# Kernel optimization log

Hardware: AMD Instinct MI355X
Metric: run time of the kernel (lower is better)

The kernel has to match this reference:

```python
import jax, jax.numpy as jnp
import numpy as np
import math

STRIDE = 32
CTR_CLAMP = 32.0
SCALE_CLAMP = math.log(1000.0 / 16)  # DEFAULT_SCALE_CLAMP
CONF_THRESH = 0.05
NMS_THRESH = 0.6
TOPK = 1000
NUM_CLASSES = 80
CLASS_OFFSET = 1.0e5  # separates classes so one IoU pass == per-class NMS


def setup_inputs() -> dict:
    key = jax.random.key(0)
    k1, k2 = jax.random.split(key)
    fmp_h, fmp_w = 100, 100
    A = 5
    M = fmp_h * fmp_w * A  # 50000 candidates
    cls_pred = jax.random.normal(k1, (M, NUM_CLASSES), dtype=jnp.float32)
    reg_pred = jax.random.normal(k2, (M, 4), dtype=jnp.float32)
    anchor_size = jnp.array([[32, 32], [64, 64], [128, 128], [256, 256], [512, 512]], dtype=jnp.float32)
    return {"cls_pred": cls_pred, "reg_pred": reg_pred, "anchor_size": anchor_size,
            "fmp_h": fmp_h, "fmp_w": fmp_w}


def _generate_anchors(anchor_size, fmp_h, fmp_w):
    # anchors laid out as [H*W, A, 4] -> [M, 4], matching torch.meshgrid order
    ys, xs = jnp.meshgrid(jnp.arange(fmp_h, dtype=jnp.float32),
                          jnp.arange(fmp_w, dtype=jnp.float32), indexing="ij")
    xy = (jnp.stack([xs, ys], axis=-1).reshape(-1, 2) + 0.5) * STRIDE  # [HW, 2]
    A = anchor_size.shape[0]
    anchor_xy = jnp.repeat(xy[:, None, :], A, axis=1)                   # [HW, A, 2]
    anchor_wh = jnp.broadcast_to(anchor_size[None], (xy.shape[0], A, 2))
    return jnp.concatenate([anchor_xy, anchor_wh], axis=-1).reshape(-1, 4)  # [M, 4]


def _decode_boxes(anchors, reg):
    # anchors/reg: [K, 4] (cx, cy, w, h) / (dx, dy, dw, dh)
    ctr_off = jnp.clip(reg[:, :2] * anchors[:, 2:], -CTR_CLAMP, CTR_CLAMP)
    ctr_xy = anchors[:, :2] + ctr_off
    wh = anchors[:, 2:] * jnp.exp(jnp.minimum(reg[:, 2:], SCALE_CLAMP))
    return jnp.concatenate([ctr_xy - 0.5 * wh, ctr_xy + 0.5 * wh], axis=-1)  # x1y1x2y2


def _greedy_nms_keep(boxes, valid):
    # boxes: [K, 4] already score-sorted descending; valid: [K] bool
    x1, y1, x2, y2 = boxes[:, 0], boxes[:, 1], boxes[:, 2], boxes[:, 3]
    areas = (x2 - x1) * (y2 - y1)
    xx1 = jnp.maximum(x1[:, None], x1[None, :])
    yy1 = jnp.maximum(y1[:, None], y1[None, :])
    xx2 = jnp.minimum(x2[:, None], x2[None, :])
    yy2 = jnp.minimum(y2[:, None], y2[None, :])
    inter = jnp.maximum(1e-28, xx2 - xx1) * jnp.maximum(1e-28, yy2 - yy1)
    iou = inter / (areas[:, None] + areas[None, :] - inter + 1e-14)  # [K, K]
    idxs = jnp.arange(boxes.shape[0])

    def body(i, keep):
        suppress = keep[i] & (iou[i] > NMS_THRESH) & (idxs > i)
        return keep & ~suppress

    return jax.lax.fori_loop(0, boxes.shape[0], body, valid)


def reference(cls_pred, reg_pred, anchor_size, fmp_h, fmp_w):
    anchors = _generate_anchors(anchor_size, fmp_h, fmp_w)  # [M, 4]
    probs = jax.nn.sigmoid(cls_pred)                        # [M, C]
    scores = probs.max(axis=-1)
    labels = probs.argmax(axis=-1)
    # top-k candidates (lax.top_k returns scores sorted descending)
    scores, idx = jax.lax.top_k(scores, TOPK)
    labels = labels[idx]
    reg = reg_pred[idx]
    anc = anchors[idx]
    boxes = _decode_boxes(anc, reg)                         # [K, 4] in pixels
    valid = scores >= CONF_THRESH
    # per-class NMS via class offsets (boxes of different classes never overlap)
    boxes_off = boxes + labels.astype(boxes.dtype)[:, None] * CLASS_OFFSET
    keep = _greedy_nms_keep(boxes_off, valid)
    img_w = fmp_w * STRIDE
    img_h = fmp_h * STRIDE
    scale = jnp.array([img_w, img_h, img_w, img_h], dtype=boxes.dtype)
    nboxes = jnp.clip(boxes / scale, 0.0, 1.0)
    m = keep.astype(boxes.dtype)
    return nboxes * m[:, None], scores * m, jnp.where(keep, labels, -1), keep
```

## Files before the change

### kernel.cpp

```cpp
#include <hip/hip_runtime.h>
#include <math.h>

#define NCLS 80
#define TOPK 1000
#define NWORDS 16
#define CAND_CAP 4096

__device__ __forceinline__ float sigmoid_np(float x) {
  float e = (float)exp(-(double)x);
  return 1.0f / (1.0f + e);
}
__device__ __forceinline__ float exp_np(float x) { return (float)exp((double)x); }

__device__ __forceinline__ unsigned fkey(float s) {
  unsigned u = __float_as_uint(s);
  return ((int)u < 0) ? ~u : (u | 0x80000000u);
}

__device__ __forceinline__ void agg_add(unsigned* h, unsigned bin, bool pred) {
  unsigned long long rem = __ballot(pred);
  const int lane = threadIdx.x & 63;
  while (rem) {
    int leader = __ffsll(rem) - 1;
    unsigned lb = (unsigned)__shfl((int)bin, leader, 64);
    unsigned long long m = __ballot(pred && bin == lb);
    if (lane == leader) atomicAdd(&h[lb], (unsigned)__popcll(m));
    rem &= ~m;
  }
}

__global__ void k_zero(unsigned* __restrict__ p, int nwords) {
  int i = blockIdx.x * 256 + threadIdx.x;
  if (i < nwords) p[i] = 0u;
}

__launch_bounds__(1024)
__global__ void k_score(const float* __restrict__ cls, float* __restrict__ scores,
                        int* __restrict__ labels, unsigned* __restrict__ ghist1, int M) {
  __shared__ unsigned h1[4096];
  const int t = threadIdx.x;
  #pragma unroll
  for (int k = 0; k < 4; ++k) h1[t + 1024 * k] = 0u;
  __syncthreads();

  int gid = blockIdx.x * 1024 + t;
  int anchor = gid >> 2;
  int q = gid & 3;
  bool act = anchor < M;
  float lv[20];
  float best = -3.4e38f; int bc = 0;
  if (act) {
    const float4* row = reinterpret_cast<const float4*>(cls) + (size_t)anchor * (NCLS / 4);
    #pragma unroll
    for (int k = 0; k < 5; ++k) {
      float4 v = row[q + 4 * k];
      int cbase = (q + 4 * k) * 4;
      lv[4 * k + 0] = v.x; lv[4 * k + 1] = v.y; lv[4 * k + 2] = v.z; lv[4 * k + 3] = v.w;
      if (v.x > best) { best = v.x; bc = cbase + 0; }
      if (v.y > best) { best = v.y; bc = cbase + 1; }
      if (v.z > best) { best = v.z; bc = cbase + 2; }
      if (v.w > best) { best = v.w; bc = cbase + 3; }
    }
  } else {
    #pragma unroll
    for (int k = 0; k < 20; ++k) lv[k] = -3.4e38f;
  }
  #pragma unroll
  for (int d = 1; d < 4; d <<= 1) {
    float ob = __shfl_xor(best, d, 64);
    int oc = __shfl_xor(bc, d, 64);
    if (ob > best || (ob == best && oc < bc)) { best = ob; bc = oc; }
  }
  float s = sigmoid_np(best);
  float sp = s * (1.0f - s);
  float band = (s < 1.0f && sp > 0.0f) ? (4.8e-7f / sp) : 3.4e38f;
  float thresh = best - band;
  int cclose = 1 << 30;
  #pragma unroll
  for (int k = 0; k < 5; ++k) {
    #pragma unroll
    for (int j = 0; j < 4; ++j) {
      int c = (q + 4 * k) * 4 + j;
      if (lv[4 * k + j] >= thresh && c < cclose) cclose = c;
    }
  }
  #pragma unroll
  for (int d = 1; d < 4; d <<= 1) {
    int oc = __shfl_xor(cclose, d, 64);
    if (oc < cclose) cclose = oc;
  }
  int lab = bc;
  if (act && cclose < bc && q == 0) {
    float bp = -1.0f; int bl = 0;
    for (int c = 0; c < NCLS; ++c) {
      float p = sigmoid_np(cls[(size_t)anchor * NCLS + c]);
      if (p > bp) { bp = p; bl = c; }
    }
    lab = bl;
  }
  if (act && q == 0) {
    scores[anchor] = s;
    labels[anchor] = lab;
  }
  agg_add(h1, fkey(s) >> 20, act && q == 0);
  __syncthreads();
  #pragma unroll
  for (int k = 0; k < 4; ++k) {
    unsigned c = h1[t + 1024 * k];
    if (c) atomicAdd(&ghist1[t + 1024 * k], c);
  }
}

__launch_bounds__(1024)
__global__ void k_hist2(const unsigned* __restrict__ ghist1, const float* __restrict__ scores,
                        unsigned* __restrict__ ghist2, unsigned* __restrict__ gmeta, int M) {
  __shared__ unsigned chunks[1024];
  __shared__ int sB1; __shared__ unsigned sAb;
  const int t = threadIdx.x;
  unsigned hb0 = ghist1[4 * t], hb1 = ghist1[4 * t + 1],
           hb2 = ghist1[4 * t + 2], hb3 = ghist1[4 * t + 3];
  chunks[t] = hb0 + hb1 + hb2 + hb3;
  __syncthreads();
  for (int d = 1; d < 1024; d <<= 1) {
    unsigned v = chunks[t] + ((t + d < 1024) ? chunks[t + d] : 0u);
    __syncthreads();
    chunks[t] = v;
    __syncthreads();
  }
  {
    unsigned ssc = chunks[t];
    unsigned ssn = (t + 1 < 1024) ? chunks[t + 1] : 0u;
    if (ssc >= (unsigned)TOPK && ssn < (unsigned)TOPK) {
      unsigned hb[4] = {hb0, hb1, hb2, hb3};
      unsigned run = ssn;
      for (int b = 3; b >= 0; --b) {
        run += hb[b];
        if (run >= (unsigned)TOPK) { sB1 = 4 * t + b; sAb = run - hb[b]; break; }
      }
    }
  }
  __syncthreads();
  const unsigned B1 = (unsigned)sB1;
  if (blockIdx.x == 0 && t == 0) { gmeta[0] = B1; gmeta[1] = sAb; }

  int base = (blockIdx.x * 1024 + t) * 4;
  if (base + 3 < M) {
    float4 v = *reinterpret_cast<const float4*>(scores + base);
    unsigned k0 = fkey(v.x), k1 = fkey(v.y), k2 = fkey(v.z), k3 = fkey(v.w);
    if ((k0 >> 20) == B1) atomicAdd(&ghist2[(k0 >> 8) & 0xFFFu], 1u);
    if ((k1 >> 20) == B1) atomicAdd(&ghist2[(k1 >> 8) & 0xFFFu], 1u);
    if ((k2 >> 20) == B1) atomicAdd(&ghist2[(k2 >> 8) & 0xFFFu], 1u);
    if ((k3 >> 20) == B1) atomicAdd(&ghist2[(k3 >> 8) & 0xFFFu], 1u);
  } else {
    for (int j = base; j < M; ++j) {
      unsigned k0 = fkey(scores[j]);
      if ((k0 >> 20) == B1) atomicAdd(&ghist2[(k0 >> 8) & 0xFFFu], 1u);
    }
  }
}

__launch_bounds__(1024)
__global__ void k_compact(const unsigned* __restrict__ ghist2, const unsigned* __restrict__ gmeta,
                          const float* __restrict__ scores,
                          unsigned long long* __restrict__ cand, unsigned* __restrict__ gcount,
                          int M) {
  __shared__ unsigned chunks[1024];
  __shared__ int sB2;
  __shared__ unsigned wcnt[16];
  __shared__ unsigned sbase;
  const int t = threadIdx.x;
  const unsigned B1 = gmeta[0], nAb = gmeta[1];
  unsigned hb0 = ghist2[4 * t], hb1 = ghist2[4 * t + 1],
           hb2 = ghist2[4 * t + 2], hb3 = ghist2[4 * t + 3];
  chunks[t] = hb0 + hb1 + hb2 + hb3;
  __syncthreads();
  for (int d = 1; d < 1024; d <<= 1) {
    unsigned v = chunks[t] + ((t + d < 1024) ? chunks[t + d] : 0u);
    __syncthreads();
    chunks[t] = v;
    __syncthreads();
  }
  {
    unsigned ssc = nAb + chunks[t];
    unsigned ssn = nAb + ((t + 1 < 1024) ? chunks[t + 1] : 0u);
    if (ssc >= (unsigned)TOPK && ssn < (unsigned)TOPK) {
      unsigned hb[4] = {hb0, hb1, hb2, hb3};
      unsigned run = ssn;
      for (int b = 3; b >= 0; --b) {
        run += hb[b];
        if (run >= (unsigned)TOPK) { sB2 = 4 * t + b; break; }
      }
    }
  }
  __syncthreads();
  const unsigned T = (B1 << 20) | ((unsigned)sB2 << 8);

  int base = (blockIdx.x * 1024 + t) * 4;
  unsigned keys[4]; int idxs[4]; int np = 0;
  #pragma unroll
  for (int j = 0; j < 4; ++j) {
    int i = base + j;
    if (i < M) {
      unsigned key = fkey(scores[i]);
      if (key >= T) { keys[np] = key; idxs[np] = i; ++np; }
    }
  }
  const int lane = t & 63, wid = t >> 6;
  int sc = np;
  #pragma unroll
  for (int d = 1; d < 64; d <<= 1) {
    int o = __shfl_up(sc, d, 64);
    if (lane >= d) sc += o;
  }
  if (lane == 63) wcnt[wid] = (unsigned)sc;
  __syncthreads();
  if (t == 0) {
    unsigned acc = 0;
    for (int w = 0; w < 16; ++w) { unsigned v = wcnt[w]; wcnt[w] = acc; acc += v; }
    sbase = acc ? atomicAdd(gcount, acc) : 0u;
  }
  __syncthreads();
  unsigned pos = sbase + wcnt[wid] + (unsigned)(sc - np);
  for (int j = 0; j < np; ++j) {
    if (pos < (unsigned)CAND_CAP)
      cand[pos] = ((unsigned long long)keys[j] << 32) | (unsigned)(~(unsigned)idxs[j]);
    ++pos;
  }
}

__launch_bounds__(1024)
__global__ void k_rank(const unsigned long long* __restrict__ cand, const unsigned* __restrict__ gcount,
                       const int* __restrict__ labels, const float* __restrict__ reg,
                       const float* __restrict__ asz, const int* __restrict__ pW, int A,
                       float* __restrict__ sel_score, int* __restrict__ sel_label,
                       float* __restrict__ boxes, float* __restrict__ areas,
                       float* __restrict__ obox) {
  __shared__ unsigned long long ck[CAND_CAP];
  const int t = threadIdx.x;
  unsigned n = *gcount; if (n > (unsigned)CAND_CAP) n = (unsigned)CAND_CAP;
  for (int i = t; i < CAND_CAP; i += 1024) ck[i] = (i < (int)n) ? cand[i] : 0ull;
  __syncthreads();
  for (int c = t; c < (int)n; c += 1024) {
    unsigned long long my = ck[c];
    int r = 0;
    for (int j = 0; j < (int)n; ++j) r += (ck[j] > my);
    if (r < TOPK) {
      unsigned key = (unsigned)(my >> 32);
      unsigned u = (key & 0x80000000u) ? (key ^ 0x80000000u) : ~key;
      float scv = __uint_as_float(u);
      int idx = (int)(~(unsigned)my);
      int lab = labels[idx];
      int W = *pW;
      int a = idx % A;
      int cell = idx / A;
      int x = cell % W;
      int y = cell / W;
      float aw = asz[a * 2 + 0], ah = asz[a * 2 + 1];
      float ax = ((float)x + 0.5f) * 32.0f;
      float ay = ((float)y + 0.5f) * 32.0f;
      float4 rg = *reinterpret_cast<const float4*>(reg + (size_t)idx * 4);
      float offx = fminf(fmaxf(rg.x * aw, -32.0f), 32.0f);
      float offy = fminf(fmaxf(rg.y * ah, -32.0f), 32.0f);
      float cx = ax + offx, cy = ay + offy;
      const float SC = 4.135166556742356f;
      float bw = aw * exp_np(fminf(rg.z, SC));
      float bh = ah * exp_np(fminf(rg.w, SC));
      float x1 = cx - 0.5f * bw, y1 = cy - 0.5f * bh;
      float x2 = cx + 0.5f * bw, y2 = cy + 0.5f * bh;
      float off = (float)lab * 100000.0f;
      float ox1 = x1 + off, oy1 = y1 + off, ox2 = x2 + off, oy2 = y2 + off;
      sel_score[r] = scv; sel_label[r] = lab;
      boxes[r * 4 + 0] = x1; boxes[r * 4 + 1] = y1;
      boxes[r * 4 + 2] = x2; boxes[r * 4 + 3] = y2;
      obox[0 * 1024 + r] = ox1; obox[1 * 1024 + r] = oy1;
      obox[2 * 1024 + r] = ox2; obox[3 * 1024 + r] = oy2;
      areas[r] = (ox2 - ox1) * (oy2 - oy1);
    }
  }
}

__launch_bounds__(256)
__global__ void k_mask(const float* __restrict__ obox, const float* __restrict__ areas,
                       unsigned long long* __restrict__ maskC) {
  __shared__ float so0[1024], so1[1024], so2[1024], so3[1024], sa[1024];
  const int t = threadIdx.x;
  int g = blockIdx.x * 256 + t;
  int c = g >> 10, j = g & 1023;
  for (int idx = t; idx < 1024; idx += 256) {
    so0[idx] = obox[idx];        so1[idx] = obox[1024 + idx];
    so2[idx] = obox[2048 + idx]; so3[idx] = obox[3072 + idx];
    sa[idx] = areas[idx];
  }
  __syncthreads();
  if (j >= TOPK) { maskC[c * 1024 + j] = 0ull; return; }
  float x1j = so0[j], y1j = so1[j], x2j = so2[j], y2j = so3[j];
  float aj = sa[j];
  unsigned long long bits = 0ull;
  int i0 = c * 64;
  for (int ii = 0; ii < 64; ++ii) {
    int i = i0 + ii;
    if (i < TOPK && i < j) {
      float xx1 = fmaxf(so0[i], x1j);
      float yy1 = fmaxf(so1[i], y1j);
      float xx2 = fminf(so2[i], x2j);
      float yy2 = fminf(so3[i], y2j);
      float inter = fmaxf(1e-28f, xx2 - xx1) * fmaxf(1e-28f, yy2 - yy1);
      float uni = sa[i] + aj - inter + 1e-14f;
      float iou = inter / uni;
      if (iou > 0.6f) bits |= (1ull << ii);
    }
  }
  maskC[c * 1024 + j] = bits;
}

__launch_bounds__(512, 1)
__global__ void k_nms(const unsigned long long* __restrict__ maskC,
                      const float* __restrict__ sel_score, const int* __restrict__ sel_label,
                      const float* __restrict__ boxes,
                      const int* __restrict__ pW, const int* __restrict__ pH,
                      float* __restrict__ out) {
  __shared__ unsigned long long sm[16 * 16 * 64];
  __shared__ float ssc[1024];
  __shared__ unsigned long long kwS[16];
  const int tid = threadIdx.x;
  const int wv = tid >> 6, lane = tid & 63;

  {
    int pair = 0;
    #pragma unroll
    for (int f = 0; f < 16; ++f) {
      #pragma unroll
      for (int g = f; g < 16; ++g) {
        if ((pair & 7) == wv)
          sm[(f * 16 + g) * 64 + lane] = maskC[f * 1024 + g * 64 + lane];
        ++pair;
      }
    }
  }
  for (int i = tid; i < 1024; i += 512)
    ssc[i] = (i < TOPK) ? sel_score[i] : 0.0f;
  __syncthreads();

  if (tid < 64) {
    unsigned long long supp[16];
    #pragma unroll
    for (int f = 0; f < 16; ++f) supp[f] = 0ull;
    #pragma unroll
    for (int f = 0; f < 16; ++f) {
      unsigned long long ct = sm[(f * 16 + f) * 64 + lane];
      unsigned long long w[16];
      #pragma unroll
      for (int g = f + 1; g < 16; ++g) w[g] = sm[(f * 16 + g) * 64 + lane];
      int r = f * 64 + lane;
      unsigned long long valid = __ballot((r < TOPK) && (ssc[r] >= 0.05f));
      unsigned long long sup_any = __ballot(ct != 0ull);
      unsigned long long avail = valid & ~supp[f];
      unsigned long long kwf = 0ull;
      while (avail) {
        unsigned long long fs = avail & sup_any;
        if (!fs) { kwf |= avail; break; }
        int i = __ffsll((long long)fs) - 1;
        unsigned long long below = (1ull << i) - 1ull;
        kwf |= avail & below;
        kwf |= (1ull << i);
        unsigned long long vict = __ballot(((ct >> i) & 1ull) != 0ull);
        avail &= ~vict;
        avail &= ~(below | (1ull << i));
      }
      if (lane == 0) kwS[f] = kwf;
      #pragma unroll
      for (int g = f + 1; g < 16; ++g)
        supp[g] |= __ballot((w[g] & kwf) != 0ull);
    }
  }
  __syncthreads();

  float sw = (float)(*pW * 32);
  float sh = (float)(*pH * 32);
  const float4* b4 = reinterpret_cast<const float4*>(boxes);
  for (int r = tid; r < TOPK; r += 512) {
    bool kp = (kwS[r >> 6] >> (r & 63)) & 1ull;
    float m = kp ? 1.0f : 0.0f;
    float4 b = b4[r];
    float b0 = fminf(fmaxf(b.x / sw, 0.0f), 1.0f) * m;
    float b1 = fminf(fmaxf(b.y / sh, 0.0f), 1.0f) * m;
    float b2 = fminf(fmaxf(b.z / sw, 0.0f), 1.0f) * m;
    float b3 = fminf(fmaxf(b.w / sh, 0.0f), 1.0f) * m;
    out[r * 4 + 0] = b0; out[r * 4 + 1] = b1;
    out[r * 4 + 2] = b2; out[r * 4 + 3] = b3;
    out[TOPK * 4 + r] = ssc[r] * m;
    out[TOPK * 5 + r] = kp ? (float)sel_label[r] : -1.0f;
    out[TOPK * 6 + r] = m;
  }
}

extern "C" void kernel_launch(void* const* d_in, const int* in_sizes, int n_in,
                              void* d_out, int out_size, void* d_ws, size_t ws_size,
                              hipStream_t stream) {
  const float* cls = (const float*)d_in[0];
  const float* reg = (const float*)d_in[1];
  const float* asz = (const float*)d_in[2];
  const int* pH = (const int*)d_in[3];
  const int* pW = (const int*)d_in[4];
  int M = in_sizes[0] / NCLS;
  int A = in_sizes[2] / 2;

  char* ws = (char*)d_ws;
  size_t off = 0;
  auto alloc = [&](size_t bytes) { size_t o = off; off = (off + bytes + 255) & ~(size_t)255; return o; };
  size_t o_h1    = alloc(4096 * sizeof(unsigned));
  size_t o_h2    = alloc(4096 * sizeof(unsigned));
  size_t o_misc  = alloc(256);
  size_t zero_end = off;
  size_t o_cand  = alloc((size_t)CAND_CAP * sizeof(unsigned long long));
  size_t o_sc    = alloc((size_t)M * sizeof(float));
  size_t o_lb    = alloc((size_t)M * sizeof(int));
  size_t o_ssc   = alloc(1024 * sizeof(float));
  size_t o_slb   = alloc(1024 * sizeof(int));
  size_t o_box   = alloc((size_t)TOPK * 4 * sizeof(float));
  size_t o_area  = alloc(1024 * sizeof(float));
  size_t o_obox  = alloc(4 * 1024 * sizeof(float));
  size_t o_mask  = alloc((size_t)NWORDS * 1024 * sizeof(unsigned long long));
  (void)ws_size; (void)out_size; (void)n_in;

  int zwords = (int)(zero_end / 4);
  k_zero<<<(zwords + 255) / 256, 256, 0, stream>>>((unsigned*)ws, zwords);

  int nblk_score = (M * 4 + 1023) / 1024;
  k_score<<<nblk_score, 1024, 0, stream>>>(
      cls, (float*)(ws + o_sc), (int*)(ws + o_lb), (unsigned*)(ws + o_h1), M);

  int nblk_scan = ((M + 3) / 4 + 1023) / 1024;
  k_hist2<<<nblk_scan, 1024, 0, stream>>>(
      (const unsigned*)(ws + o_h1), (const float*)(ws + o_sc),
      (unsigned*)(ws + o_h2), (unsigned*)(ws + o_misc + 8), M);
  k_compact<<<nblk_scan, 1024, 0, stream>>>(
      (const unsigned*)(ws + o_h2), (const unsigned*)(ws + o_misc + 8),
      (const float*)(ws + o_sc),
      (unsigned long long*)(ws + o_cand), (unsigned*)(ws + o_misc), M);
  k_rank<<<1, 1024, 0, stream>>>(
      (const unsigned long long*)(ws + o_cand), (const unsigned*)(ws + o_misc),
      (const int*)(ws + o_lb), reg, asz, pW, A,
      (float*)(ws + o_ssc), (int*)(ws + o_slb),
      (float*)(ws + o_box), (float*)(ws + o_area), (float*)(ws + o_obox));
  k_mask<<<(NWORDS * 1024) / 256, 256, 0, stream>>>(
      (const float*)(ws + o_obox), (const float*)(ws + o_area),
      (unsigned long long*)(ws + o_mask));
  k_nms<<<1, 512, 0, stream>>>(
      (const unsigned long long*)(ws + o_mask),
      (const float*)(ws + o_ssc), (const int*)(ws + o_slb),
      (const float*)(ws + o_box), pW, pH, (float*)d_out);
}
```

Baseline: 77.39 us.

## Fuse second-pass histogram, compaction and ranking into one single-block select kernel

Replaces the separate k_hist2, k_compact and k_rank kernels with one 1024-thread single-block kernel. It builds the second-level histogram in shared memory, compacts candidates into shared memory with wave-aggregated atomics, and ranks them there. This removes two kernel launches and the global histogram, candidate and metadata round trips. In exchange, one block must scan all 50000 scores twice, which gives up grid-wide parallelism. The change also restructures k_mask to 16 blocks of 1024 threads and has k_nms copy the full mask with vectorized loads.

```diff
diff --git a/kernel.cpp b/kernel.cpp
--- a/kernel.cpp
+++ b/kernel.cpp
@@ -3,7 +3,6 @@
 
 #define NCLS 80
 #define TOPK 1000
-#define NWORDS 16
 #define CAND_CAP 4096
 
 __device__ __forceinline__ float sigmoid_np(float x) {
@@ -112,20 +111,34 @@
 }
 
 __launch_bounds__(1024)
-__global__ void k_hist2(const unsigned* __restrict__ ghist1, const float* __restrict__ scores,
-                        unsigned* __restrict__ ghist2, unsigned* __restrict__ gmeta, int M) {
+__global__ void k_select(const unsigned* __restrict__ ghist1, const float* __restrict__ scores,
+                         const int* __restrict__ labels, const float* __restrict__ reg,
+                         const float* __restrict__ asz, const int* __restrict__ pW,
+                         int M, int A,
+                         float* __restrict__ sel_score, int* __restrict__ sel_label,
+                         float* __restrict__ boxes, float* __restrict__ areas,
+                         float* __restrict__ obox) {
+  __shared__ unsigned hist2[4096];
   __shared__ unsigned chunks[1024];
-  __shared__ int sB1; __shared__ unsigned sAb;
+  __shared__ unsigned long long ck[CAND_CAP];
+  __shared__ int sB1, sB2;
+  __shared__ unsigned sAb, scnt;
   const int t = threadIdx.x;
+  const int lane = t & 63;
+  const int M4 = M >> 2;
+  const float4* s4 = reinterpret_cast<const float4*>(scores);
+
+  #pragma unroll
+  for (int k = 0; k < 4; ++k) hist2[t + 1024 * k] = 0u;
+  if (t == 0) scnt = 0u;
+
   unsigned hb0 = ghist1[4 * t], hb1 = ghist1[4 * t + 1],
            hb2 = ghist1[4 * t + 2], hb3 = ghist1[4 * t + 3];
   chunks[t] = hb0 + hb1 + hb2 + hb3;
   __syncthreads();
   for (int d = 1; d < 1024; d <<= 1) {
     unsigned v = chunks[t] + ((t + d < 1024) ? chunks[t + d] : 0u);
-    __syncthreads();
-    chunks[t] = v;
-    __syncthreads();
+    __syncthreads(); chunks[t] = v; __syncthreads();
   }
   {
     unsigned ssc = chunks[t];
@@ -141,50 +154,31 @@
   }
   __syncthreads();
   const unsigned B1 = (unsigned)sB1;
-  if (blockIdx.x == 0 && t == 0) { gmeta[0] = B1; gmeta[1] = sAb; }
-
-  int base = (blockIdx.x * 1024 + t) * 4;
-  if (base + 3 < M) {
-    float4 v = *reinterpret_cast<const float4*>(scores + base);
+  const unsigned nAb = sAb;
+
+  for (int i = t; i < M4; i += 1024) {
+    float4 v = s4[i];
     unsigned k0 = fkey(v.x), k1 = fkey(v.y), k2 = fkey(v.z), k3 = fkey(v.w);
-    if ((k0 >> 20) == B1) atomicAdd(&ghist2[(k0 >> 8) & 0xFFFu], 1u);
-    if ((k1 >> 20) == B1) atomicAdd(&ghist2[(k1 >> 8) & 0xFFFu], 1u);
-    if ((k2 >> 20) == B1) atomicAdd(&ghist2[(k2 >> 8) & 0xFFFu], 1u);
-    if ((k3 >> 20) == B1) atomicAdd(&ghist2[(k3 >> 8) & 0xFFFu], 1u);
-  } else {
-    for (int j = base; j < M; ++j) {
-      unsigned k0 = fkey(scores[j]);
-      if ((k0 >> 20) == B1) atomicAdd(&ghist2[(k0 >> 8) & 0xFFFu], 1u);
-    }
-  }
-}
-
-__launch_bounds__(1024)
-__global__ void k_compact(const unsigned* __restrict__ ghist2, const unsigned* __restrict__ gmeta,
-                          const float* __restrict__ scores,
-                          unsigned long long* __restrict__ cand, unsigned* __restrict__ gcount,
-                          int M) {
-  __shared__ unsigned chunks[1024];
-  __shared__ int sB2;
-  __shared__ unsigned wcnt[16];
-  __shared__ unsigned sbase;
-  const int t = threadIdx.x;
-  const unsigned B1 = gmeta[0], nAb = gmeta[1];
-  unsigned hb0 = ghist2[4 * t], hb1 = ghist2[4 * t + 1],
-           hb2 = ghist2[4 * t + 2], hb3 = ghist2[4 * t + 3];
-  chunks[t] = hb0 + hb1 + hb2 + hb3;
+    if ((k0 >> 20) == B1) atomicAdd(&hist2[(k0 >> 8) & 0xFFFu], 1u);
+    if ((k1 >> 20) == B1) atomicAdd(&hist2[(k1 >> 8) & 0xFFFu], 1u);
+    if ((k2 >> 20) == B1) atomicAdd(&hist2[(k2 >> 8) & 0xFFFu], 1u);
+    if ((k3 >> 20) == B1) atomicAdd(&hist2[(k3 >> 8) & 0xFFFu], 1u);
+  }
+  __syncthreads();
+
+  unsigned g0 = hist2[4 * t], g1 = hist2[4 * t + 1],
+           g2 = hist2[4 * t + 2], g3 = hist2[4 * t + 3];
+  chunks[t] = g0 + g1 + g2 + g3;
   __syncthreads();
   for (int d = 1; d < 1024; d <<= 1) {
     unsigned v = chunks[t] + ((t + d < 1024) ? chunks[t + d] : 0u);
-    __syncthreads();
-    chunks[t] = v;
-    __syncthreads();
+    __syncthreads(); chunks[t] = v; __syncthreads();
   }
   {
     unsigned ssc = nAb + chunks[t];
     unsigned ssn = nAb + ((t + 1 < 1024) ? chunks[t + 1] : 0u);
     if (ssc >= (unsigned)TOPK && ssn < (unsigned)TOPK) {
-      unsigned hb[4] = {hb0, hb1, hb2, hb3};
+      unsigned hb[4] = {g0, g1, g2, g3};
       unsigned run = ssn;
       for (int b = 3; b >= 0; --b) {
         run += hb[b];
@@ -195,56 +189,33 @@
   __syncthreads();
   const unsigned T = (B1 << 20) | ((unsigned)sB2 << 8);
 
-  int base = (blockIdx.x * 1024 + t) * 4;
-  unsigned keys[4]; int idxs[4]; int np = 0;
-  #pragma unroll
-  for (int j = 0; j < 4; ++j) {
-    int i = base + j;
-    if (i < M) {
-      unsigned key = fkey(scores[i]);
-      if (key >= T) { keys[np] = key; idxs[np] = i; ++np; }
-    }
-  }
-  const int lane = t & 63, wid = t >> 6;
-  int sc = np;
-  #pragma unroll
-  for (int d = 1; d < 64; d <<= 1) {
-    int o = __shfl_up(sc, d, 64);
-    if (lane >= d) sc += o;
-  }
-  if (lane == 63) wcnt[wid] = (unsigned)sc;
-  __syncthreads();
-  if (t == 0) {
-    unsigned acc = 0;
-    for (int w = 0; w < 16; ++w) { unsigned v = wcnt[w]; wcnt[w] = acc; acc += v; }
-    sbase = acc ? atomicAdd(gcount, acc) : 0u;
-  }
-  __syncthreads();
-  unsigned pos = sbase + wcnt[wid] + (unsigned)(sc - np);
-  for (int j = 0; j < np; ++j) {
-    if (pos < (unsigned)CAND_CAP)
-      cand[pos] = ((unsigned long long)keys[j] << 32) | (unsigned)(~(unsigned)idxs[j]);
-    ++pos;
-  }
-}
-
-__launch_bounds__(1024)
-__global__ void k_rank(const unsigned long long* __restrict__ cand, const unsigned* __restrict__ gcount,
-                       const int* __restrict__ labels, const float* __restrict__ reg,
-                       const float* __restrict__ asz, const int* __restrict__ pW, int A,
-                       float* __restrict__ sel_score, int* __restrict__ sel_label,
-                       float* __restrict__ boxes, float* __restrict__ areas,
-                       float* __restrict__ obox) {
-  __shared__ unsigned long long ck[CAND_CAP];
-  const int t = threadIdx.x;
-  unsigned n = *gcount; if (n > (unsigned)CAND_CAP) n = (unsigned)CAND_CAP;
-  for (int i = t; i < CAND_CAP; i += 1024) ck[i] = (i < (int)n) ? cand[i] : 0ull;
-  __syncthreads();
-  for (int c = t; c < (int)n; c += 1024) {
-    unsigned long long my = ck[c];
+  for (int i = t; i < M; i += 1024) {
+    unsigned key = fkey(scores[i]);
+    bool pred = key >= T;
+    unsigned long long m = __ballot(pred);
+    if (m) {
+      int leader = __ffsll(m) - 1;
+      unsigned base = 0;
+      if (lane == leader) base = atomicAdd(&scnt, (unsigned)__popcll(m));
+      base = (unsigned)__shfl((int)base, leader, 64);
+      if (pred) {
+        unsigned p = base + (unsigned)__popcll(m & ((1ull << lane) - 1ull));
+        if (p < (unsigned)CAND_CAP)
+          ck[p] = ((unsigned long long)key << 32) | (unsigned)(~(unsigned)i);
+      }
+    }
+  }
+  __syncthreads();
+  unsigned n = scnt; if (n > (unsigned)CAND_CAP) n = (unsigned)CAND_CAP;
+
+  for (int cc = 0; cc < CAND_CAP; cc += 1024) {
+    if ((unsigned)cc >= n) break;
+    int c = cc + t;
+    bool actv = (unsigned)c < n;
+    unsigned long long my = actv ? ck[c] : 0ull;
     int r = 0;
     for (int j = 0; j < (int)n; ++j) r += (ck[j] > my);
-    if (r < TOPK) {
+    if (actv && r < TOPK) {
       unsigned key = (unsigned)(my >> 32);
       unsigned u = (key & 0x80000000u) ? (key ^ 0x80000000u) : ~key;
       float scv = __uint_as_float(u);
@@ -279,66 +250,64 @@
   }
 }
 
-__launch_bounds__(256)
+__launch_bounds__(1024)
 __global__ void k_mask(const float* __restrict__ obox, const float* __restrict__ areas,
                        unsigned long long* __restrict__ maskC) {
   __shared__ float so0[1024], so1[1024], so2[1024], so3[1024], sa[1024];
   const int t = threadIdx.x;
-  int g = blockIdx.x * 256 + t;
-  int c = g >> 10, j = g & 1023;
-  for (int idx = t; idx < 1024; idx += 256) {
-    so0[idx] = obox[idx];        so1[idx] = obox[1024 + idx];
-    so2[idx] = obox[2048 + idx]; so3[idx] = obox[3072 + idx];
-    sa[idx] = areas[idx];
-  }
-  __syncthreads();
-  if (j >= TOPK) { maskC[c * 1024 + j] = 0ull; return; }
-  float x1j = so0[j], y1j = so1[j], x2j = so2[j], y2j = so3[j];
-  float aj = sa[j];
+  const int c = blockIdx.x, j = t;
+  so0[t] = obox[t];        so1[t] = obox[1024 + t];
+  so2[t] = obox[2048 + t]; so3[t] = obox[3072 + t];
+  sa[t] = areas[t];
+  __syncthreads();
   unsigned long long bits = 0ull;
-  int i0 = c * 64;
-  for (int ii = 0; ii < 64; ++ii) {
-    int i = i0 + ii;
-    if (i < TOPK && i < j) {
-      float xx1 = fmaxf(so0[i], x1j);
-      float yy1 = fmaxf(so1[i], y1j);
-      float xx2 = fminf(so2[i], x2j);
-      float yy2 = fminf(so3[i], y2j);
-      float inter = fmaxf(1e-28f, xx2 - xx1) * fmaxf(1e-28f, yy2 - yy1);
-      float uni = sa[i] + aj - inter + 1e-14f;
-      float iou = inter / uni;
-      if (iou > 0.6f) bits |= (1ull << ii);
+  if (j < TOPK) {
+    float x1j = so0[j], y1j = so1[j], x2j = so2[j], y2j = so3[j];
+    float aj = sa[j];
+    int i0 = c * 64;
+    for (int ii = 0; ii < 64; ++ii) {
+      int i = i0 + ii;
+      if (i < TOPK && i < j) {
+        float xx1 = fmaxf(so0[i], x1j);
+        float yy1 = fmaxf(so1[i], y1j);
+        float xx2 = fminf(so2[i], x2j);
+        float yy2 = fminf(so3[i], y2j);
+        float inter = fmaxf(1e-28f, xx2 - xx1) * fmaxf(1e-28f, yy2 - yy1);
+        float uni = sa[i] + aj - inter + 1e-14f;
+        float iou = inter / uni;
+        if (iou > 0.6f) bits |= (1ull << ii);
+      }
     }
   }
   maskC[c * 1024 + j] = bits;
 }
 
-__launch_bounds__(512, 1)
+__launch_bounds__(512)
 __global__ void k_nms(const unsigned long long* __restrict__ maskC,
                       const float* __restrict__ sel_score, const int* __restrict__ sel_label,
                       const float* __restrict__ boxes,
                       const int* __restrict__ pW, const int* __restrict__ pH,
                       float* __restrict__ out) {
-  __shared__ unsigned long long sm[16 * 16 * 64];
+  __shared__ unsigned long long sm[16 * 1024];
   __shared__ float ssc[1024];
   __shared__ unsigned long long kwS[16];
   const int tid = threadIdx.x;
-  const int wv = tid >> 6, lane = tid & 63;
+  const int lane = tid & 63;
 
   {
-    int pair = 0;
-    #pragma unroll
-    for (int f = 0; f < 16; ++f) {
-      #pragma unroll
-      for (int g = f; g < 16; ++g) {
-        if ((pair & 7) == wv)
-          sm[(f * 16 + g) * 64 + lane] = maskC[f * 1024 + g * 64 + lane];
-        ++pair;
-      }
-    }
-  }
-  for (int i = tid; i < 1024; i += 512)
+    const float4* g4 = reinterpret_cast<const float4*>(maskC);
+    float4* s4 = reinterpret_cast<float4*>(sm);
+    float4 v[16];
+    #pragma unroll
+    for (int k = 0; k < 16; ++k) v[k] = g4[tid + k * 512];
+    #pragma unroll
+    for (int k = 0; k < 16; ++k) s4[tid + k * 512] = v[k];
+  }
+  #pragma unroll
+  for (int k = 0; k < 2; ++k) {
+    int i = tid + k * 512;
     ssc[i] = (i < TOPK) ? sel_score[i] : 0.0f;
+  }
   __syncthreads();
 
   if (tid < 64) {
@@ -347,10 +316,7 @@
     for (int f = 0; f < 16; ++f) supp[f] = 0ull;
     #pragma unroll
     for (int f = 0; f < 16; ++f) {
-      unsigned long long ct = sm[(f * 16 + f) * 64 + lane];
-      unsigned long long w[16];
-      #pragma unroll
-      for (int g = f + 1; g < 16; ++g) w[g] = sm[(f * 16 + g) * 64 + lane];
+      unsigned long long ct = sm[f * 1024 + f * 64 + lane];
       int r = f * 64 + lane;
       unsigned long long valid = __ballot((r < TOPK) && (ssc[r] >= 0.05f));
       unsigned long long sup_any = __ballot(ct != 0ull);
@@ -370,7 +336,7 @@
       if (lane == 0) kwS[f] = kwf;
       #pragma unroll
       for (int g = f + 1; g < 16; ++g)
-        supp[g] |= __ballot((w[g] & kwf) != 0ull);
+        supp[g] |= __ballot((sm[f * 1024 + g * 64 + lane] & kwf) != 0ull);
     }
   }
   __syncthreads();
@@ -408,42 +374,27 @@
   char* ws = (char*)d_ws;
   size_t off = 0;
   auto alloc = [&](size_t bytes) { size_t o = off; off = (off + bytes + 255) & ~(size_t)255; return o; };
-  size_t o_h1    = alloc(4096 * sizeof(unsigned));
-  size_t o_h2    = alloc(4096 * sizeof(unsigned));
-  size_t o_misc  = alloc(256);
-  size_t zero_end = off;
-  size_t o_cand  = alloc((size_t)CAND_CAP * sizeof(unsigned long long));
-  size_t o_sc    = alloc((size_t)M * sizeof(float));
-  size_t o_lb    = alloc((size_t)M * sizeof(int));
-  size_t o_ssc   = alloc(1024 * sizeof(float));
-  size_t o_slb   = alloc(1024 * sizeof(int));
-  size_t o_box   = alloc((size_t)TOPK * 4 * sizeof(float));
-  size_t o_area  = alloc(1024 * sizeof(float));
-  size_t o_obox  = alloc(4 * 1024 * sizeof(float));
-  size_t o_mask  = alloc((size_t)NWORDS * 1024 * sizeof(unsigned long long));
+  size_t o_h1   = alloc(4096 * sizeof(unsigned));
+  size_t o_sc   = alloc((size_t)M * sizeof(float));
+  size_t o_lb   = alloc((size_t)M * sizeof(int));
+  size_t o_ssc  = alloc(1024 * sizeof(float));
+  size_t o_slb  = alloc(1024 * sizeof(int));
+  size_t o_box  = alloc((size_t)TOPK * 4 * sizeof(float));
+  size_t o_area = alloc(1024 * sizeof(float));
+  size_t o_obox = alloc(4 * 1024 * sizeof(float));
+  size_t o_mask = alloc((size_t)16 * 1024 * sizeof(unsigned long long));
   (void)ws_size; (void)out_size; (void)n_in;
 
-  int zwords = (int)(zero_end / 4);
-  k_zero<<<(zwords + 255) / 256, 256, 0, stream>>>((unsigned*)ws, zwords);
-
+  k_zero<<<16, 256, 0, stream>>>((unsigned*)(ws + o_h1), 4096);
   int nblk_score = (M * 4 + 1023) / 1024;
   k_score<<<nblk_score, 1024, 0, stream>>>(
       cls, (float*)(ws + o_sc), (int*)(ws + o_lb), (unsigned*)(ws + o_h1), M);
-
-  int nblk_scan = ((M + 3) / 4 + 1023) / 1024;
-  k_hist2<<<nblk_scan, 1024, 0, stream>>>(
-      (const unsigned*)(ws + o_h1), (const float*)(ws + o_sc),
-      (unsigned*)(ws + o_h2), (unsigned*)(ws + o_misc + 8), M);
-  k_compact<<<nblk_scan, 1024, 0, stream>>>(
-      (const unsigned*)(ws + o_h2), (const unsigned*)(ws + o_misc + 8),
-      (const float*)(ws + o_sc),
-      (unsigned long long*)(ws + o_cand), (unsigned*)(ws + o_misc), M);
-  k_rank<<<1, 1024, 0, stream>>>(
-      (const unsigned long long*)(ws + o_cand), (const unsigned*)(ws + o_misc),
-      (const int*)(ws + o_lb), reg, asz, pW, A,
+  k_select<<<1, 1024, 0, stream>>>(
+      (const unsigned*)(ws + o_h1), (const float*)(ws + o_sc), (const int*)(ws + o_lb),
+      reg, asz, pW, M, A,
       (float*)(ws + o_ssc), (int*)(ws + o_slb),
       (float*)(ws + o_box), (float*)(ws + o_area), (float*)(ws + o_obox));
-  k_mask<<<(NWORDS * 1024) / 256, 256, 0, stream>>>(
+  k_mask<<<16, 1024, 0, stream>>>(
       (const float*)(ws + o_obox), (const float*)(ws + o_area),
       (unsigned long long*)(ws + o_mask));
   k_nms<<<1, 512, 0, stream>>>(
```

Result: slower. 87.43 us (+13.0%).
